# Kernel tuning notes

Hardware: AMD Instinct MI355X
Metric: run time of the kernel (lower is better)

## Reference

```python
import jax, jax.numpy as jnp
import numpy as np

B = 16384          # batch
F = 26             # num sparse features
D = 13             # num dense features
V = 100000         # vocab per sparse feature
E = 16             # embedding size
HID = [400, 400, 400]
DNN_IN = F * E + D  # 429


def setup_inputs() -> dict:
    key = jax.random.key(0)
    ks = jax.random.split(key, 16)
    inp = {}
    inp["x_sparse"] = jax.random.randint(ks[0], (B, F), 0, V, dtype=jnp.int32)
    inp["x_dense"] = jax.random.uniform(ks[1], (B, D), dtype=jnp.float32)
    # embedding tables (stacked across features; all vocabs equal)
    inp["emb1"] = jax.random.normal(ks[2], (F, V, 1), dtype=jnp.float32) * 0.0001
    inp["emb2"] = jax.random.normal(ks[3], (F, V, E), dtype=jnp.float32) * 0.0001
    inp["w_dense"] = jax.random.normal(ks[4], (D, 1), dtype=jnp.float32) * 0.0001
    inp["bias"] = jnp.zeros((1,), dtype=jnp.float32)
    dims = [DNN_IN] + HID
    for i in range(3):
        inp[f"dnn_w{i}"] = jax.random.normal(ks[5 + i], (dims[i], dims[i + 1]), dtype=jnp.float32) * 0.02
        inp[f"dnn_b{i}"] = jnp.zeros((dims[i + 1],), dtype=jnp.float32)
    inp["final_w"] = jax.random.normal(ks[9], (HID[-1], 1), dtype=jnp.float32) * 0.02
    return inp


def reference(x_sparse, x_dense, emb1, emb2, w_dense, bias,
              dnn_w0, dnn_b0, dnn_w1, dnn_b1, dnn_w2, dnn_b2, final_w):
    f_idx = jnp.arange(F)[None, :]                      # [1, F]
    # FM linear: per-feature 1-d embedding lookup, summed over features
    e1 = emb1[f_idx, x_sparse, 0]                       # [B, F]
    linear_sparse = jnp.sum(e1, axis=-1, keepdims=True)  # [B, 1]
    linear_dense = x_dense @ w_dense                    # [B, 1]
    logit = linear_sparse + linear_dense
    # FM second order: square-of-sum minus sum-of-square
    fm = emb2[f_idx, x_sparse]                          # [B, F, E]
    s = jnp.sum(fm, axis=1)                             # [B, E]
    cross = 0.5 * jnp.sum(s * s - jnp.sum(fm * fm, axis=1), axis=-1, keepdims=True)  # [B, 1]
    logit = logit + cross
    # DNN
    h = jnp.concatenate([fm.reshape(x_sparse.shape[0], F * E), x_dense], axis=-1)  # [B, F*E+D]
    h = jax.nn.relu(h @ dnn_w0 + dnn_b0)
    h = jax.nn.relu(h @ dnn_w1 + dnn_b1)
    h = jax.nn.relu(h @ dnn_w2 + dnn_b2)
    logit = logit + h @ final_w                         # [B, 1]
    return jax.nn.sigmoid(logit + bias)
```

## Files before the change

kernel.cpp:

```cpp
#include <hip/hip_runtime.h>
#include <hip/hip_bf16.h>
#include <math.h>

#define BATCH 16384
#define NF 26
#define ND 13
#define VOC 100000
#define KP0 448
#define KP1 416

typedef __bf16 bf16x8 __attribute__((ext_vector_type(8)));
typedef float f32x4 __attribute__((ext_vector_type(4)));
using bf16 = __hip_bfloat16;

__device__ __forceinline__ void gload_lds16(const void* g, void* l) {
  __builtin_amdgcn_global_load_lds(
      (const __attribute__((address_space(1))) void*)g,
      (__attribute__((address_space(3))) void*)l, 16, 0, 0);
}

__global__ void prep_kernel(const float* __restrict__ w0, const float* __restrict__ w1,
                            const float* __restrict__ w2, bf16* __restrict__ wt0,
                            bf16* __restrict__ wt1, bf16* __restrict__ wt2) {
  int bid = blockIdx.x, tid = threadIdx.x;
  const float* W; bf16* Wt; int K, KP, idx;
  if (bid < 728)       { W = w0; Wt = wt0; K = 429; KP = KP0; idx = bid * 256 + tid; }
  else if (bid < 1404) { W = w1; Wt = wt1; K = 400; KP = KP1; idx = (bid - 728) * 256 + tid; }
  else                 { W = w2; Wt = wt2; K = 400; KP = KP1; idx = (bid - 1404) * 256 + tid; }
  int k = idx % KP, n = idx / KP;
  float v = (k < K && n < 400) ? W[(size_t)k * 400 + n] : 0.f;
  Wt[idx] = __float2bfloat16(v);
}

__global__ __launch_bounds__(256) void gather_fm_kernel(
    const int* __restrict__ xs, const float* __restrict__ xd,
    const float* __restrict__ emb1, const float* __restrict__ emb2,
    const float* __restrict__ wd, const float* __restrict__ bias,
    bf16* __restrict__ h0, float* __restrict__ partial) {
  int gid = blockIdx.x * blockDim.x + threadIdx.x;
  int b = gid >> 6;
  int lane = threadIdx.x & 63;
  int fsub = lane >> 4;
  int e = lane & 15;
  float s_acc = 0.f, sq_acc = 0.f, lin = 0.f;
#pragma unroll
  for (int it = 0; it < 7; ++it) {
    int f = it * 4 + fsub;
    if (f < NF) {
      int idx = xs[b * NF + f];
      float v = emb2[((size_t)(f * VOC + idx)) * 16 + e];
      h0[(size_t)b * KP0 + f * 16 + e] = __float2bfloat16(v);
      s_acc += v;
      sq_acc += v * v;
      if (e == 0) lin += emb1[(size_t)f * VOC + idx];
    }
  }
  if (lane < 32) {
    float v = 0.f;
    if (lane < ND) { v = xd[b * ND + lane]; lin += v * wd[lane]; }
    h0[(size_t)b * KP0 + 416 + lane] = __float2bfloat16(v);
  }
  float s_tot = s_acc;
  s_tot += __shfl_xor(s_tot, 16);
  s_tot += __shfl_xor(s_tot, 32);
  float r0 = s_tot * s_tot;
  float r1 = sq_acc;
  float r2 = lin;
#pragma unroll
  for (int off = 1; off < 64; off <<= 1) {
    r0 += __shfl_xor(r0, off);
    r1 += __shfl_xor(r1, off);
    r2 += __shfl_xor(r2, off);
  }
  if (lane == 0) {
    float cross = 0.5f * (r0 * 0.25f - r1);
    partial[b] = bias[0] + r2 + cross;
  }
}

template <int KP, bool FINAL>
__global__ __launch_bounds__(256) void mlp3_kernel(
    const bf16* __restrict__ A, const bf16* __restrict__ Wt,
    const float* __restrict__ bias, bf16* __restrict__ outH,
    const float* __restrict__ fw, float* __restrict__ dotb) {
  constexpr int NK = KP / 32;
  __shared__ __align__(16) bf16 slab[2][208 * 32];
  const int bid = blockIdx.x;
  const int ch = bid & 1;
  const int tid = threadIdx.x, w = tid >> 6, lane = tid & 63;
  const int r = lane & 15, g = lane >> 4;
  const int row0 = (bid >> 1) * 64 + w * 16;
  const int ncol0 = ch * 208;
  const char* wbase = (const char*)(Wt + (size_t)ncol0 * KP);

  auto stage = [&](int buf, int k) {
#pragma unroll
    for (int rd = 0; rd < 4; ++rd) {
      int c = rd * 256 + tid;
      if (c < 832) {
        int n = c >> 2, j = c & 3;
        int kc = j ^ ((n >> 1) & 3);
        gload_lds16(wbase + (size_t)n * (KP * 2) + k * 64 + kc * 16,
                    (char*)&slab[buf][0] + (rd * 256 + w * 64) * 16);
      }
    }
  };

  const char* Ab = (const char*)(A + (size_t)(row0 + r) * KP) + g * 16;
  bf16x8 aNext = *(const bf16x8*)(Ab);
  stage(0, 0);
  __syncthreads();

  f32x4 acc[13];
#pragma unroll
  for (int nt = 0; nt < 13; ++nt) acc[nt] = (f32x4){0.f, 0.f, 0.f, 0.f};

  const int chunkoff = ((g ^ ((r >> 1) & 3)) << 4);
  int cur = 0;
  for (int k = 0; k < NK; ++k) {
    bf16x8 aCur = aNext;
    if (k + 1 < NK) {
      aNext = *(const bf16x8*)(Ab + (k + 1) * 64);
      stage(cur ^ 1, k + 1);
    }
    const char* sb = (const char*)&slab[cur][0] + r * 64 + chunkoff;
#pragma unroll
    for (int nt = 0; nt < 13; ++nt) {
      bf16x8 b = *(const bf16x8*)(sb + nt * 1024);
      acc[nt] = __builtin_amdgcn_mfma_f32_16x16x32_bf16(aCur, b, acc[nt], 0, 0, 0);
    }
    __syncthreads();
    cur ^= 1;
  }

  if (!FINAL) {
#pragma unroll
    for (int nt = 0; nt < 13; ++nt) {
      int col = ncol0 + nt * 16 + r;
      bool live = (col < 400);
      float bv = live ? bias[col] : 0.f;
#pragma unroll
      for (int q = 0; q < 4; ++q) {
        float v = live ? fmaxf(acc[nt][q] + bv, 0.f) : 0.f;
        outH[(size_t)(row0 + g * 4 + q) * KP1 + col] = __float2bfloat16(v);
      }
    }
  } else {
    float pr[4] = {0.f, 0.f, 0.f, 0.f};
#pragma unroll
    for (int nt = 0; nt < 13; ++nt) {
      int col = ncol0 + nt * 16 + r;
      if (col < 400) {
        float bv = bias[col], fv = fw[col];
#pragma unroll
        for (int q = 0; q < 4; ++q)
          pr[q] += fmaxf(acc[nt][q] + bv, 0.f) * fv;
      }
    }
#pragma unroll
    for (int q = 0; q < 4; ++q) {
      pr[q] += __shfl_xor(pr[q], 1);
      pr[q] += __shfl_xor(pr[q], 2);
      pr[q] += __shfl_xor(pr[q], 4);
      pr[q] += __shfl_xor(pr[q], 8);
    }
    if (r < 4) {
      float v = (r == 0) ? pr[0] : (r == 1) ? pr[1] : (r == 2) ? pr[2] : pr[3];
      dotb[(size_t)ch * BATCH + row0 + g * 4 + r] = v;
    }
  }
}

__global__ void finish_kernel(const float* __restrict__ partial,
                              const float* __restrict__ dotb,
                              float* __restrict__ out) {
  int i = blockIdx.x * 256 + threadIdx.x;
  if (i < BATCH) {
    float x = partial[i] + dotb[i] + dotb[i + BATCH];
    out[i] = 1.f / (1.f + expf(-x));
  }
}

extern "C" void kernel_launch(void* const* d_in, const int* in_sizes, int n_in,
                              void* d_out, int out_size, void* d_ws, size_t ws_size,
                              hipStream_t stream) {
  const int* xs = (const int*)d_in[0];
  const float* xd = (const float*)d_in[1];
  const float* emb1 = (const float*)d_in[2];
  const float* emb2 = (const float*)d_in[3];
  const float* wd = (const float*)d_in[4];
  const float* bias = (const float*)d_in[5];
  const float* w0 = (const float*)d_in[6];
  const float* b0 = (const float*)d_in[7];
  const float* w1 = (const float*)d_in[8];
  const float* b1 = (const float*)d_in[9];
  const float* w2 = (const float*)d_in[10];
  const float* b2 = (const float*)d_in[11];
  const float* fw = (const float*)d_in[12];
  float* out = (float*)d_out;

  char* ws = (char*)d_ws;
  float* partial = (float*)(ws + 0);
  float* dotb    = (float*)(ws + 65536);
  bf16* wt0 = (bf16*)(ws + 196608);
  bf16* wt1 = (bf16*)(ws + 569344);
  bf16* wt2 = (bf16*)(ws + 915456);
  bf16* h0  = (bf16*)(ws + 1261568);
  bf16* h1  = (bf16*)(ws + 15941632);
  bf16* h2  = h0;

  prep_kernel<<<2080, 256, 0, stream>>>(w0, w1, w2, wt0, wt1, wt2);
  gather_fm_kernel<<<BATCH / 4, 256, 0, stream>>>(xs, xd, emb1, emb2, wd, bias, h0, partial);

  mlp3_kernel<KP0, false><<<512, 256, 0, stream>>>(h0, wt0, b0, h1, nullptr, nullptr);
  mlp3_kernel<KP1, false><<<512, 256, 0, stream>>>(h1, wt1, b1, h2, nullptr, nullptr);
  mlp3_kernel<KP1, true><<<512, 256, 0, stream>>>(h2, wt2, b2, nullptr, fw, dotb);

  finish_kernel<<<BATCH / 256, 256, 0, stream>>>(partial, dotb, out);
}
```

Measured before the change: 80.01 us.

## Merge prep into gather, retile MLP waves by column, fuse sigmoid into final layer

The weight-transpose prep kernel and the embedding gather kernel become one launch, with the work split by block index. In the middle MLP layers each wave now covers all 64 rows of the block and only 3-4 of the 13 column tiles. Each LDS B fragment is therefore reused across 4 MFMAs instead of being read by every wave separately. The final layer covers all 416 columns per block of 32 rows, does the dot-product reduction through LDS, and applies the sigmoid in place. This removes the dotb buffer and the finish kernel. The cost is higher register use per wave (16 accumulators plus 4 A fragments), a larger LDS slab in fin_kernel, and wave 0 carrying 4 column tiles against 3 for the others.

Measured after the change: 90.31 us. 1.13x slower.

```diff
diff --git a/kernel.cpp b/kernel.cpp
--- a/kernel.cpp
+++ b/kernel.cpp
@@ -19,27 +19,28 @@
       (__attribute__((address_space(3))) void*)l, 16, 0, 0);
 }
 
-__global__ void prep_kernel(const float* __restrict__ w0, const float* __restrict__ w1,
-                            const float* __restrict__ w2, bf16* __restrict__ wt0,
-                            bf16* __restrict__ wt1, bf16* __restrict__ wt2) {
-  int bid = blockIdx.x, tid = threadIdx.x;
-  const float* W; bf16* Wt; int K, KP, idx;
-  if (bid < 728)       { W = w0; Wt = wt0; K = 429; KP = KP0; idx = bid * 256 + tid; }
-  else if (bid < 1404) { W = w1; Wt = wt1; K = 400; KP = KP1; idx = (bid - 728) * 256 + tid; }
-  else                 { W = w2; Wt = wt2; K = 400; KP = KP1; idx = (bid - 1404) * 256 + tid; }
-  int k = idx % KP, n = idx / KP;
-  float v = (k < K && n < 400) ? W[(size_t)k * 400 + n] : 0.f;
-  Wt[idx] = __float2bfloat16(v);
-}
-
-__global__ __launch_bounds__(256) void gather_fm_kernel(
+__global__ __launch_bounds__(256) void prep_gather_kernel(
+    const float* __restrict__ w0, const float* __restrict__ w1,
+    const float* __restrict__ w2, bf16* __restrict__ wt0,
+    bf16* __restrict__ wt1, bf16* __restrict__ wt2,
     const int* __restrict__ xs, const float* __restrict__ xd,
     const float* __restrict__ emb1, const float* __restrict__ emb2,
-    const float* __restrict__ wd, const float* __restrict__ bias,
+    const float* __restrict__ wd, const float* __restrict__ biasp,
     bf16* __restrict__ h0, float* __restrict__ partial) {
-  int gid = blockIdx.x * blockDim.x + threadIdx.x;
+  const int bid = blockIdx.x, tid = threadIdx.x;
+  if (bid < 2080) {
+    const float* W; bf16* Wt; int K, KP, idx;
+    if (bid < 728)       { W = w0; Wt = wt0; K = 429; KP = KP0; idx = bid * 256 + tid; }
+    else if (bid < 1404) { W = w1; Wt = wt1; K = 400; KP = KP1; idx = (bid - 728) * 256 + tid; }
+    else                 { W = w2; Wt = wt2; K = 400; KP = KP1; idx = (bid - 1404) * 256 + tid; }
+    int k = idx % KP, n = idx / KP;
+    float v = (k < K && n < 400) ? W[(size_t)k * 400 + n] : 0.f;
+    Wt[idx] = __float2bfloat16(v);
+    return;
+  }
+  int gid = (bid - 2080) * 256 + tid;
   int b = gid >> 6;
-  int lane = threadIdx.x & 63;
+  int lane = tid & 63;
   int fsub = lane >> 4;
   int e = lane & 15;
   float s_acc = 0.f, sq_acc = 0.f, lin = 0.f;
@@ -74,22 +75,21 @@
   }
   if (lane == 0) {
     float cross = 0.5f * (r0 * 0.25f - r1);
-    partial[b] = bias[0] + r2 + cross;
-  }
-}
-
-template <int KP, bool FINAL>
-__global__ __launch_bounds__(256) void mlp3_kernel(
+    partial[b] = biasp[0] + r2 + cross;
+  }
+}
+
+template <int KP>
+__global__ __launch_bounds__(256) void mid_kernel(
     const bf16* __restrict__ A, const bf16* __restrict__ Wt,
-    const float* __restrict__ bias, bf16* __restrict__ outH,
-    const float* __restrict__ fw, float* __restrict__ dotb) {
+    const float* __restrict__ bias, bf16* __restrict__ outH) {
   constexpr int NK = KP / 32;
   __shared__ __align__(16) bf16 slab[2][208 * 32];
   const int bid = blockIdx.x;
   const int ch = bid & 1;
   const int tid = threadIdx.x, w = tid >> 6, lane = tid & 63;
   const int r = lane & 15, g = lane >> 4;
-  const int row0 = (bid >> 1) * 64 + w * 16;
+  const int row0 = (bid >> 1) * 64;
   const int ncol0 = ch * 208;
   const char* wbase = (const char*)(Wt + (size_t)ncol0 * KP);
 
@@ -106,78 +106,168 @@
     }
   };
 
+  const int ntc = (w == 0) ? 4 : 3;
+  const int tb0 = (w == 0) ? 0 : 4 + (w - 1) * 3;
+
   const char* Ab = (const char*)(A + (size_t)(row0 + r) * KP) + g * 16;
-  bf16x8 aNext = *(const bf16x8*)(Ab);
+  const size_t rtStride = (size_t)16 * KP * 2;
+  bf16x8 aNext[4];
+#pragma unroll
+  for (int rt = 0; rt < 4; ++rt)
+    aNext[rt] = *(const bf16x8*)(Ab + rt * rtStride);
   stage(0, 0);
   __syncthreads();
 
-  f32x4 acc[13];
-#pragma unroll
-  for (int nt = 0; nt < 13; ++nt) acc[nt] = (f32x4){0.f, 0.f, 0.f, 0.f};
+  f32x4 acc[4][4];
+#pragma unroll
+  for (int rt = 0; rt < 4; ++rt)
+#pragma unroll
+    for (int nt = 0; nt < 4; ++nt) acc[rt][nt] = (f32x4){0.f, 0.f, 0.f, 0.f};
 
   const int chunkoff = ((g ^ ((r >> 1) & 3)) << 4);
   int cur = 0;
   for (int k = 0; k < NK; ++k) {
-    bf16x8 aCur = aNext;
+    bf16x8 aCur[4];
+#pragma unroll
+    for (int rt = 0; rt < 4; ++rt) aCur[rt] = aNext[rt];
     if (k + 1 < NK) {
-      aNext = *(const bf16x8*)(Ab + (k + 1) * 64);
+#pragma unroll
+      for (int rt = 0; rt < 4; ++rt)
+        aNext[rt] = *(const bf16x8*)(Ab + (k + 1) * 64 + rt * rtStride);
       stage(cur ^ 1, k + 1);
     }
     const char* sb = (const char*)&slab[cur][0] + r * 64 + chunkoff;
 #pragma unroll
-    for (int nt = 0; nt < 13; ++nt) {
-      bf16x8 b = *(const bf16x8*)(sb + nt * 1024);
-      acc[nt] = __builtin_amdgcn_mfma_f32_16x16x32_bf16(aCur, b, acc[nt], 0, 0, 0);
-    }
+    for (int nt = 0; nt < 4; ++nt)
+      if (nt < ntc) {
+        bf16x8 bfr = *(const bf16x8*)(sb + (tb0 + nt) * 1024);
+#pragma unroll
+        for (int rt = 0; rt < 4; ++rt)
+          acc[rt][nt] = __builtin_amdgcn_mfma_f32_16x16x32_bf16(aCur[rt], bfr, acc[rt][nt], 0, 0, 0);
+      }
     __syncthreads();
     cur ^= 1;
   }
 
-  if (!FINAL) {
-#pragma unroll
-    for (int nt = 0; nt < 13; ++nt) {
-      int col = ncol0 + nt * 16 + r;
+#pragma unroll
+  for (int nt = 0; nt < 4; ++nt)
+    if (nt < ntc) {
+      int col = ncol0 + (tb0 + nt) * 16 + r;
       bool live = (col < 400);
       float bv = live ? bias[col] : 0.f;
 #pragma unroll
-      for (int q = 0; q < 4; ++q) {
-        float v = live ? fmaxf(acc[nt][q] + bv, 0.f) : 0.f;
-        outH[(size_t)(row0 + g * 4 + q) * KP1 + col] = __float2bfloat16(v);
-      }
-    }
-  } else {
-    float pr[4] = {0.f, 0.f, 0.f, 0.f};
-#pragma unroll
-    for (int nt = 0; nt < 13; ++nt) {
-      int col = ncol0 + nt * 16 + r;
+      for (int rt = 0; rt < 4; ++rt)
+#pragma unroll
+        for (int q = 0; q < 4; ++q) {
+          float v = live ? fmaxf(acc[rt][nt][q] + bv, 0.f) : 0.f;
+          outH[(size_t)(row0 + rt * 16 + g * 4 + q) * KP1 + col] = __float2bfloat16(v);
+        }
+    }
+}
+
+__global__ __launch_bounds__(256) void fin_kernel(
+    const bf16* __restrict__ A, const bf16* __restrict__ Wt,
+    const float* __restrict__ bias, const float* __restrict__ fw,
+    const float* __restrict__ partial, float* __restrict__ out) {
+  constexpr int KP = KP1, NK = KP1 / 32;
+  __shared__ __align__(16) bf16 slab[2][416 * 32];
+  __shared__ float dr[128];
+  const int bid = blockIdx.x;
+  const int tid = threadIdx.x, w = tid >> 6, lane = tid & 63;
+  const int r = lane & 15, g = lane >> 4;
+  const int row0 = bid * 32;
+
+  auto stage = [&](int buf, int k) {
+#pragma unroll
+    for (int rd = 0; rd < 7; ++rd) {
+      int c = rd * 256 + tid;
+      if (c < 1664) {
+        int n = c >> 2, j = c & 3;
+        int kc = j ^ ((n >> 1) & 3);
+        gload_lds16((const char*)Wt + (size_t)n * (KP * 2) + k * 64 + kc * 16,
+                    (char*)&slab[buf][0] + (rd * 256 + w * 64) * 16);
+      }
+    }
+  };
+
+  const int ntc = (w < 2) ? 7 : 6;
+  const int tb0 = (w < 2) ? w * 7 : 14 + (w - 2) * 6;
+
+  const char* Ab = (const char*)(A + (size_t)(row0 + r) * KP) + g * 16;
+  const size_t rtStride = (size_t)16 * KP * 2;
+  bf16x8 aNext[2];
+#pragma unroll
+  for (int rt = 0; rt < 2; ++rt)
+    aNext[rt] = *(const bf16x8*)(Ab + rt * rtStride);
+  stage(0, 0);
+  __syncthreads();
+
+  f32x4 acc[2][7];
+#pragma unroll
+  for (int rt = 0; rt < 2; ++rt)
+#pragma unroll
+    for (int nt = 0; nt < 7; ++nt) acc[rt][nt] = (f32x4){0.f, 0.f, 0.f, 0.f};
+
+  const int chunkoff = ((g ^ ((r >> 1) & 3)) << 4);
+  int cur = 0;
+  for (int k = 0; k < NK; ++k) {
+    bf16x8 aCur[2];
+#pragma unroll
+    for (int rt = 0; rt < 2; ++rt) aCur[rt] = aNext[rt];
+    if (k + 1 < NK) {
+#pragma unroll
+      for (int rt = 0; rt < 2; ++rt)
+        aNext[rt] = *(const bf16x8*)(Ab + (k + 1) * 64 + rt * rtStride);
+      stage(cur ^ 1, k + 1);
+    }
+    const char* sb = (const char*)&slab[cur][0] + r * 64 + chunkoff;
+#pragma unroll
+    for (int nt = 0; nt < 7; ++nt)
+      if (nt < ntc) {
+        bf16x8 bfr = *(const bf16x8*)(sb + (tb0 + nt) * 1024);
+#pragma unroll
+        for (int rt = 0; rt < 2; ++rt)
+          acc[rt][nt] = __builtin_amdgcn_mfma_f32_16x16x32_bf16(aCur[rt], bfr, acc[rt][nt], 0, 0, 0);
+      }
+    __syncthreads();
+    cur ^= 1;
+  }
+
+  float pr[2][4] = {{0.f, 0.f, 0.f, 0.f}, {0.f, 0.f, 0.f, 0.f}};
+#pragma unroll
+  for (int nt = 0; nt < 7; ++nt)
+    if (nt < ntc) {
+      int col = (tb0 + nt) * 16 + r;
       if (col < 400) {
         float bv = bias[col], fv = fw[col];
 #pragma unroll
-        for (int q = 0; q < 4; ++q)
-          pr[q] += fmaxf(acc[nt][q] + bv, 0.f) * fv;
-      }
-    }
+        for (int rt = 0; rt < 2; ++rt)
+#pragma unroll
+          for (int q = 0; q < 4; ++q)
+            pr[rt][q] += fmaxf(acc[rt][nt][q] + bv, 0.f) * fv;
+      }
+    }
+#pragma unroll
+  for (int rt = 0; rt < 2; ++rt)
 #pragma unroll
     for (int q = 0; q < 4; ++q) {
-      pr[q] += __shfl_xor(pr[q], 1);
-      pr[q] += __shfl_xor(pr[q], 2);
-      pr[q] += __shfl_xor(pr[q], 4);
-      pr[q] += __shfl_xor(pr[q], 8);
-    }
-    if (r < 4) {
-      float v = (r == 0) ? pr[0] : (r == 1) ? pr[1] : (r == 2) ? pr[2] : pr[3];
-      dotb[(size_t)ch * BATCH + row0 + g * 4 + r] = v;
-    }
-  }
-}
-
-__global__ void finish_kernel(const float* __restrict__ partial,
-                              const float* __restrict__ dotb,
-                              float* __restrict__ out) {
-  int i = blockIdx.x * 256 + threadIdx.x;
-  if (i < BATCH) {
-    float x = partial[i] + dotb[i] + dotb[i + BATCH];
-    out[i] = 1.f / (1.f + expf(-x));
+      pr[rt][q] += __shfl_xor(pr[rt][q], 1);
+      pr[rt][q] += __shfl_xor(pr[rt][q], 2);
+      pr[rt][q] += __shfl_xor(pr[rt][q], 4);
+      pr[rt][q] += __shfl_xor(pr[rt][q], 8);
+    }
+  if (r < 4) {
+#pragma unroll
+    for (int rt = 0; rt < 2; ++rt) {
+      float v = (r == 0) ? pr[rt][0] : (r == 1) ? pr[rt][1]
+              : (r == 2) ? pr[rt][2] : pr[rt][3];
+      dr[w * 32 + rt * 16 + g * 4 + r] = v;
+    }
+  }
+  __syncthreads();
+  if (tid < 32) {
+    float x = partial[row0 + tid] + dr[tid] + dr[32 + tid] + dr[64 + tid] + dr[96 + tid];
+    out[row0 + tid] = 1.f / (1.f + expf(-x));
   }
 }
 
@@ -201,20 +291,17 @@
 
   char* ws = (char*)d_ws;
   float* partial = (float*)(ws + 0);
-  float* dotb    = (float*)(ws + 65536);
-  bf16* wt0 = (bf16*)(ws + 196608);
-  bf16* wt1 = (bf16*)(ws + 569344);
-  bf16* wt2 = (bf16*)(ws + 915456);
-  bf16* h0  = (bf16*)(ws + 1261568);
-  bf16* h1  = (bf16*)(ws + 15941632);
+  bf16* wt0 = (bf16*)(ws + 65536);
+  bf16* wt1 = (bf16*)(ws + 438272);
+  bf16* wt2 = (bf16*)(ws + 784384);
+  bf16* h0  = (bf16*)(ws + 1130496);
+  bf16* h1  = (bf16*)(ws + 15810560);
   bf16* h2  = h0;
 
-  prep_kernel<<<2080, 256, 0, stream>>>(w0, w1, w2, wt0, wt1, wt2);
-  gather_fm_kernel<<<BATCH / 4, 256, 0, stream>>>(xs, xd, emb1, emb2, wd, bias, h0, partial);
-
-  mlp3_kernel<KP0, false><<<512, 256, 0, stream>>>(h0, wt0, b0, h1, nullptr, nullptr);
-  mlp3_kernel<KP1, false><<<512, 256, 0, stream>>>(h1, wt1, b1, h2, nullptr, nullptr);
-  mlp3_kernel<KP1, true><<<512, 256, 0, stream>>>(h2, wt2, b2, nullptr, fw, dotb);
-
-  finish_kernel<<<BATCH / 256, 256, 0, stream>>>(partial, dotb, out);
-}
+  prep_gather_kernel<<<2080 + BATCH / 4, 256, 0, stream>>>(
+      w0, w1, w2, wt0, wt1, wt2, xs, xd, emb1, emb2, wd, bias, h0, partial);
+
+  mid_kernel<KP0><<<512, 256, 0, stream>>>(h0, wt0, b0, h1);
+  mid_kernel<KP1><<<512, 256, 0, stream>>>(h1, wt1, b1, h2);
+  fin_kernel<<<512, 256, 0, stream>>>(h2, wt2, b2, fw, partial, out);
+}
```

## Stage full weight column slab in LDS once and tile 128 rows per block

Applied to the files above, without the earlier changes.

The MLP GEMM kernels change tiling. Instead of double-buffering 208-column weight chunks across k-steps, each block now loads an entire 80-column slice of weights for all k into dynamic LDS once. It then computes a 128-row tile with two row-tiles per wave, reusing each B fragment across two MFMAs. Columns are split into 5 slices, with a block-index mapping that groups 8 row-chunks. This removes the per-k-step syncs and raises B reuse, at the cost of large LDS use (about 70KB per block) and unpipelined direct global A loads. dotb now holds five partials, and h2 gets its own buffer.

Result: no change. 78.77 us (-1.6%).

```diff
diff --git a/kernel.cpp b/kernel.cpp
--- a/kernel.cpp
+++ b/kernel.cpp
@@ -8,6 +8,8 @@
 #define VOC 100000
 #define KP0 448
 #define KP1 416
+#define CS 80
+#define NSL 5
 
 typedef __bf16 bf16x8 __attribute__((ext_vector_type(8)));
 typedef float f32x4 __attribute__((ext_vector_type(4)));
@@ -78,95 +80,100 @@
   }
 }
 
-template <int KP, bool FINAL>
-__global__ __launch_bounds__(256) void mlp3_kernel(
+template <int NK, bool FINAL>
+__global__ __launch_bounds__(256, 2) void gemm_kernel(
     const bf16* __restrict__ A, const bf16* __restrict__ Wt,
     const float* __restrict__ bias, bf16* __restrict__ outH,
     const float* __restrict__ fw, float* __restrict__ dotb) {
-  constexpr int NK = KP / 32;
-  __shared__ __align__(16) bf16 slab[2][208 * 32];
-  const int bid = blockIdx.x;
-  const int ch = bid & 1;
-  const int tid = threadIdx.x, w = tid >> 6, lane = tid & 63;
-  const int r = lane & 15, g = lane >> 4;
-  const int row0 = (bid >> 1) * 64 + w * 16;
-  const int ncol0 = ch * 208;
-  const char* wbase = (const char*)(Wt + (size_t)ncol0 * KP);
-
-  auto stage = [&](int buf, int k) {
-#pragma unroll
-    for (int rd = 0; rd < 4; ++rd) {
-      int c = rd * 256 + tid;
-      if (c < 832) {
-        int n = c >> 2, j = c & 3;
+  constexpr int KP = NK * 32;
+  extern __shared__ __align__(16) char smem[];
+  const int b = blockIdx.x, tid = threadIdx.x;
+  const int w = tid >> 6, lane = tid & 63, r = lane & 15, g = lane >> 4;
+  const int lane8 = b & 7, hi = b >> 3;
+  const int s = hi % NSL, mchunk = (hi / NSL) * 8 + lane8;
+  const int row0 = mchunk * 128, col0 = s * CS;
+
+  {
+    const char* wbase = (const char*)(Wt + (size_t)col0 * KP);
+    constexpr int T = NK * CS * 4;
+    constexpr int FULL = T >> 8, REM = T & 255;
+    for (int rd = 0; rd <= FULL; ++rd) {
+      if (rd < FULL || tid < REM) {
+        int c = rd * 256 + tid;
+        int kk = c / (CS * 4), rm = c - kk * (CS * 4);
+        int n = rm >> 2, j = rm & 3;
         int kc = j ^ ((n >> 1) & 3);
-        gload_lds16(wbase + (size_t)n * (KP * 2) + k * 64 + kc * 16,
-                    (char*)&slab[buf][0] + (rd * 256 + w * 64) * 16);
+        gload_lds16(wbase + (size_t)n * (KP * 2) + kk * 64 + kc * 16,
+                    smem + (rd * 256 + w * 64) * 16);
       }
     }
-  };
-
-  const char* Ab = (const char*)(A + (size_t)(row0 + r) * KP) + g * 16;
-  bf16x8 aNext = *(const bf16x8*)(Ab);
-  stage(0, 0);
+  }
   __syncthreads();
 
-  f32x4 acc[13];
-#pragma unroll
-  for (int nt = 0; nt < 13; ++nt) acc[nt] = (f32x4){0.f, 0.f, 0.f, 0.f};
-
-  const int chunkoff = ((g ^ ((r >> 1) & 3)) << 4);
-  int cur = 0;
+  const char* Ab = (const char*)(A + (size_t)(row0 + w * 32 + r) * KP) + g * 16;
+  const size_t rtS = (size_t)16 * KP * 2;
+
+  f32x4 acc[2][NSL];
+#pragma unroll
+  for (int rt = 0; rt < 2; ++rt)
+#pragma unroll
+    for (int ct = 0; ct < NSL; ++ct) acc[rt][ct] = (f32x4){0.f, 0.f, 0.f, 0.f};
+
+  const int swz = ((g ^ ((r >> 1) & 3)) << 4);
   for (int k = 0; k < NK; ++k) {
-    bf16x8 aCur = aNext;
-    if (k + 1 < NK) {
-      aNext = *(const bf16x8*)(Ab + (k + 1) * 64);
-      stage(cur ^ 1, k + 1);
-    }
-    const char* sb = (const char*)&slab[cur][0] + r * 64 + chunkoff;
-#pragma unroll
-    for (int nt = 0; nt < 13; ++nt) {
-      bf16x8 b = *(const bf16x8*)(sb + nt * 1024);
-      acc[nt] = __builtin_amdgcn_mfma_f32_16x16x32_bf16(aCur, b, acc[nt], 0, 0, 0);
-    }
-    __syncthreads();
-    cur ^= 1;
+    bf16x8 a0 = *(const bf16x8*)(Ab + k * 64);
+    bf16x8 a1 = *(const bf16x8*)(Ab + k * 64 + rtS);
+    const char* sb = smem + k * (CS * 64) + r * 64 + swz;
+#pragma unroll
+    for (int ct = 0; ct < NSL; ++ct) {
+      bf16x8 bfr = *(const bf16x8*)(sb + ct * 1024);
+      acc[0][ct] = __builtin_amdgcn_mfma_f32_16x16x32_bf16(a0, bfr, acc[0][ct], 0, 0, 0);
+      acc[1][ct] = __builtin_amdgcn_mfma_f32_16x16x32_bf16(a1, bfr, acc[1][ct], 0, 0, 0);
+    }
   }
 
   if (!FINAL) {
 #pragma unroll
-    for (int nt = 0; nt < 13; ++nt) {
-      int col = ncol0 + nt * 16 + r;
-      bool live = (col < 400);
-      float bv = live ? bias[col] : 0.f;
+    for (int ct = 0; ct < NSL; ++ct) {
+      int col = col0 + ct * 16 + r;
+      float bv = bias[col];
+#pragma unroll
+      for (int rt = 0; rt < 2; ++rt)
+#pragma unroll
+        for (int q = 0; q < 4; ++q) {
+          float v = fmaxf(acc[rt][ct][q] + bv, 0.f);
+          outH[(size_t)(row0 + w * 32 + rt * 16 + g * 4 + q) * KP1 + col] =
+              __float2bfloat16(v);
+        }
+    }
+  } else {
+    float pr[2][4] = {{0.f, 0.f, 0.f, 0.f}, {0.f, 0.f, 0.f, 0.f}};
+#pragma unroll
+    for (int ct = 0; ct < NSL; ++ct) {
+      int col = col0 + ct * 16 + r;
+      float bv = bias[col], fv = fw[col];
+#pragma unroll
+      for (int rt = 0; rt < 2; ++rt)
+#pragma unroll
+        for (int q = 0; q < 4; ++q)
+          pr[rt][q] += fmaxf(acc[rt][ct][q] + bv, 0.f) * fv;
+    }
+#pragma unroll
+    for (int rt = 0; rt < 2; ++rt)
 #pragma unroll
       for (int q = 0; q < 4; ++q) {
-        float v = live ? fmaxf(acc[nt][q] + bv, 0.f) : 0.f;
-        outH[(size_t)(row0 + g * 4 + q) * KP1 + col] = __float2bfloat16(v);
+        pr[rt][q] += __shfl_xor(pr[rt][q], 1);
+        pr[rt][q] += __shfl_xor(pr[rt][q], 2);
+        pr[rt][q] += __shfl_xor(pr[rt][q], 4);
+        pr[rt][q] += __shfl_xor(pr[rt][q], 8);
       }
-    }
-  } else {
-    float pr[4] = {0.f, 0.f, 0.f, 0.f};
-#pragma unroll
-    for (int nt = 0; nt < 13; ++nt) {
-      int col = ncol0 + nt * 16 + r;
-      if (col < 400) {
-        float bv = bias[col], fv = fw[col];
-#pragma unroll
-        for (int q = 0; q < 4; ++q)
-          pr[q] += fmaxf(acc[nt][q] + bv, 0.f) * fv;
+    if (r < 4) {
+#pragma unroll
+      for (int rt = 0; rt < 2; ++rt) {
+        float v = (r == 0) ? pr[rt][0] : (r == 1) ? pr[rt][1]
+                : (r == 2) ? pr[rt][2] : pr[rt][3];
+        dotb[(size_t)s * BATCH + row0 + w * 32 + rt * 16 + g * 4 + r] = v;
       }
-    }
-#pragma unroll
-    for (int q = 0; q < 4; ++q) {
-      pr[q] += __shfl_xor(pr[q], 1);
-      pr[q] += __shfl_xor(pr[q], 2);
-      pr[q] += __shfl_xor(pr[q], 4);
-      pr[q] += __shfl_xor(pr[q], 8);
-    }
-    if (r < 4) {
-      float v = (r == 0) ? pr[0] : (r == 1) ? pr[1] : (r == 2) ? pr[2] : pr[3];
-      dotb[(size_t)ch * BATCH + row0 + g * 4 + r] = v;
     }
   }
 }
@@ -176,7 +183,8 @@
                               float* __restrict__ out) {
   int i = blockIdx.x * 256 + threadIdx.x;
   if (i < BATCH) {
-    float x = partial[i] + dotb[i] + dotb[i + BATCH];
+    float x = partial[i] + dotb[i] + dotb[BATCH + i] + dotb[2 * BATCH + i]
+            + dotb[3 * BATCH + i] + dotb[4 * BATCH + i];
     out[i] = 1.f / (1.f + expf(-x));
   }
 }
@@ -202,19 +210,28 @@
   char* ws = (char*)d_ws;
   float* partial = (float*)(ws + 0);
   float* dotb    = (float*)(ws + 65536);
-  bf16* wt0 = (bf16*)(ws + 196608);
-  bf16* wt1 = (bf16*)(ws + 569344);
-  bf16* wt2 = (bf16*)(ws + 915456);
-  bf16* h0  = (bf16*)(ws + 1261568);
-  bf16* h1  = (bf16*)(ws + 15941632);
-  bf16* h2  = h0;
+  bf16* wt0 = (bf16*)(ws + 393216);
+  bf16* wt1 = (bf16*)(ws + 765952);
+  bf16* wt2 = (bf16*)(ws + 1112064);
+  bf16* h0  = (bf16*)(ws + 1458176);
+  bf16* h1  = (bf16*)(ws + 16138240);
+  bf16* h2  = (bf16*)(ws + 29769728);
+
+  constexpr int LDS14 = 14 * CS * 64;
+  constexpr int LDS13 = 13 * CS * 64;
+  hipFuncSetAttribute((const void*)gemm_kernel<14, false>,
+                      hipFuncAttributeMaxDynamicSharedMemorySize, LDS14);
+  hipFuncSetAttribute((const void*)gemm_kernel<13, false>,
+                      hipFuncAttributeMaxDynamicSharedMemorySize, LDS13);
+  hipFuncSetAttribute((const void*)gemm_kernel<13, true>,
+                      hipFuncAttributeMaxDynamicSharedMemorySize, LDS13);
 
   prep_kernel<<<2080, 256, 0, stream>>>(w0, w1, w2, wt0, wt1, wt2);
   gather_fm_kernel<<<BATCH / 4, 256, 0, stream>>>(xs, xd, emb1, emb2, wd, bias, h0, partial);
 
-  mlp3_kernel<KP0, false><<<512, 256, 0, stream>>>(h0, wt0, b0, h1, nullptr, nullptr);
-  mlp3_kernel<KP1, false><<<512, 256, 0, stream>>>(h1, wt1, b1, h2, nullptr, nullptr);
-  mlp3_kernel<KP1, true><<<512, 256, 0, stream>>>(h2, wt2, b2, nullptr, fw, dotb);
-
-  finish_kernel<<<BATCH / 256, 256, 0, stream>>>(partial, dotb, out);
-}
+  gemm_kernel<14, false><<<640, 256, LDS14, stream>>>(h0, wt0, b0, h1, nullptr, nullptr);
+  gemm_kernel<13, false><<<640, 256, LDS13, stream>>>(h1, wt1, b1, h2, nullptr, nullptr);
+  gemm_kernel<13, true><<<640, 256, LDS13, stream>>>(h2, wt2, b2, nullptr, fw, dotb);
+
+  finish_kernel<<<64, 256, 0, stream>>>(partial, dotb, out);
+}
```
